# Optimization experiments

Hardware: AMD Instinct MI355X
Metric: run time of the kernel (lower is better)

## Reference

```python
import jax, jax.numpy as jnp
import numpy as np

NHEAD = 8  # matches init_kwargs

M_NODES = 20000
D_MODEL = 512
N_EDGES = 640000


def setup_inputs() -> dict:
    key = jax.random.key(0)
    ks = jax.random.split(key, 8)
    sc = 1.0 / np.sqrt(D_MODEL)
    return {
        "s": jax.random.normal(ks[0], (M_NODES, D_MODEL), dtype=jnp.float32),
        "edge_index": jax.random.randint(ks[1], (2, N_EDGES), 0, M_NODES, dtype=jnp.int64),
        "Wq": jax.random.normal(ks[2], (D_MODEL, D_MODEL), dtype=jnp.float32) * sc,
        "bq": jax.random.normal(ks[3], (D_MODEL,), dtype=jnp.float32) * sc,
        "Wkv": jax.random.normal(ks[4], (2 * D_MODEL, D_MODEL), dtype=jnp.float32) * sc,
        "bkv": jax.random.normal(ks[5], (2 * D_MODEL,), dtype=jnp.float32) * sc,
        "Wo": jax.random.normal(ks[6], (D_MODEL, D_MODEL), dtype=jnp.float32) * sc,
        "bo": jax.random.normal(ks[7], (D_MODEL,), dtype=jnp.float32) * sc,
    }


def reference(s, edge_index, Wq, bq, Wkv, bkv, Wo, bo):
    M, C = s.shape
    H = NHEAD
    Dh = C // H
    scale = 1.0 / np.sqrt(Dh).astype(np.float32)

    q = (s @ Wq.T + bq).reshape(M, H, Dh)            # [M,H,Dh]
    kv = (s @ Wkv.T + bkv).reshape(M, H, 2 * Dh)     # [M,H,2Dh]
    k, v = kv[..., :Dh], kv[..., Dh:]

    src, tgt = edge_index[0], edge_index[1]

    # per-edge attention logits [E,H]
    a = jnp.einsum('ehc,ehc->eh', q[tgt], k[src]) * scale

    # segment softmax over edges sharing the same target node
    a_max = jax.ops.segment_max(a, tgt, num_segments=M)        # [M,H]
    ex = jnp.exp(a - a_max[tgt])                               # [E,H]
    denom = jax.ops.segment_sum(ex, tgt, num_segments=M)      # [M,H]
    attn = ex / denom[tgt]                                     # [E,H]

    # weighted message aggregation: scatter-sum over target nodes
    o_msg = attn[..., None] * v[src]                           # [E,H,Dh]
    o = jax.ops.segment_sum(o_msg, tgt, num_segments=M)       # [M,H,Dh]
    o = o.reshape(M, C)
    return o @ Wo.T + bo
```

## Files before the change

### kernel.cpp

```cpp
#include <hip/hip_runtime.h>
#include <cmath>

#define MN 20000
#define DM 512
#define NE 640000
#define CAP 128

typedef short bf16x8 __attribute__((ext_vector_type(8)));
typedef float f32x4 __attribute__((ext_vector_type(4)));
typedef int   i32x4 __attribute__((ext_vector_type(4)));

__device__ __forceinline__ ushort f2b(float x) {
    unsigned u = __builtin_bit_cast(unsigned, x);
    u += 0x7FFF + ((u >> 16) & 1);
    return (ushort)(u >> 16);
}
__device__ __forceinline__ float b2f(ushort b) {
    return __builtin_bit_cast(float, (unsigned)b << 16);
}

#define NS4   (MN * DM / 4)
#define NWC4  (1536 * 512 / 4)
#define NWO4  (512 * 512 / 4)
#define NB4   (1536 / 4)

__device__ __forceinline__ const float* wc_src_row(int r, const float* Wq, const float* Wkv) {
    if (r < 512) return Wq + ((size_t)r << 9);
    if (r < 1024) { int h = (r - 512) >> 6, j = (r - 512) & 63;  return Wkv + ((size_t)(h * 128 + j) << 9); }
    { int h = (r - 1024) >> 6, j = (r - 1024) & 63; return Wkv + ((size_t)(h * 128 + 64 + j) << 9); }
}

__global__ void conv_all_k(const float* __restrict__ s, const float* __restrict__ Wq,
                           const float* __restrict__ Wkv, const float* __restrict__ Wo,
                           const float* __restrict__ bq, const float* __restrict__ bkv,
                           ushort* __restrict__ s_b, ushort* __restrict__ Wc_b,
                           ushort* __restrict__ Wo_b, float* __restrict__ bc)
{
    int i = blockIdx.x * blockDim.x + threadIdx.x;
    if (i < NS4) {
        float4 v = ((const float4*)s)[i];
        ushort4 o = { f2b(v.x), f2b(v.y), f2b(v.z), f2b(v.w) };
        ((ushort4*)s_b)[i] = o;
        return;
    }
    i -= NS4;
    if (i < NWC4) {
        int e = i * 4, row = e >> 9, col = e & 511;
        float4 v = *(const float4*)(wc_src_row(row, Wq, Wkv) + col);
        ushort4 o = { f2b(v.x), f2b(v.y), f2b(v.z), f2b(v.w) };
        ((ushort4*)Wc_b)[i] = o;
        return;
    }
    i -= NWC4;
    if (i < NWO4) {
        float4 v = ((const float4*)Wo)[i];
        ushort4 o = { f2b(v.x), f2b(v.y), f2b(v.z), f2b(v.w) };
        ((ushort4*)Wo_b)[i] = o;
        return;
    }
    i -= NWO4;
    if (i < NB4) {
#pragma unroll
        for (int u = 0; u < 4; ++u) {
            int r = i * 4 + u;
            float v;
            if (r < 512) v = bq[r];
            else if (r < 1024) { int h = (r - 512) >> 6, j = (r - 512) & 63;  v = bkv[h * 128 + j]; }
            else               { int h = (r - 1024) >> 6, j = (r - 1024) & 63; v = bkv[h * 128 + 64 + j]; }
            bc[r] = v;
        }
    }
}

template<int SPLIT, bool OUTBF>
__global__ __launch_bounds__(256) void gemm_mfma(
    const ushort* __restrict__ Ah, const ushort* __restrict__ Al,
    const ushort* __restrict__ Bh, const ushort* __restrict__ Bl,
    const float* __restrict__ bias, void* __restrict__ Cout, int M, int N, int K)
{
    __shared__ ushort lds[4 * 4096];
    const int tid = threadIdx.x;
    const int row0 = blockIdx.x * 128, col0 = blockIdx.y * 128;
    const int wid = tid >> 6, l = tid & 63;
    const int wm = (wid >> 1) * 64, wn = (wid & 1) * 64;
    const int fr = l & 15, g = l >> 4;
    const int fcb = g << 4;

    f32x4 acc[4][4] = {};

    for (int k0 = 0; k0 < K; k0 += 32) {
        __syncthreads();
#pragma unroll
        for (int c = 0; c < 2; ++c) {
            const int lb  = c * 4096 + tid * 16;
            const int r   = lb >> 6;
            const int cbs = (lb & 63) ^ ((r & 6) << 3);
            const int ar  = min(row0 + r, M - 1);
            const int br  = col0 + r;
            const size_t aoff = (size_t)ar * K + k0 + (cbs >> 1);
            const size_t boff = (size_t)br * K + k0 + (cbs >> 1);
            __builtin_amdgcn_global_load_lds(
                (const __attribute__((address_space(1))) void*)(Ah + aoff),
                (__attribute__((address_space(3))) void*)&lds[0 * 4096 + (lb >> 1)], 16, 0, 0);
            __builtin_amdgcn_global_load_lds(
                (const __attribute__((address_space(1))) void*)(Bh + boff),
                (__attribute__((address_space(3))) void*)&lds[1 * 4096 + (lb >> 1)], 16, 0, 0);
            if (SPLIT == 3) {
                __builtin_amdgcn_global_load_lds(
                    (const __attribute__((address_space(1))) void*)(Al + aoff),
                    (__attribute__((address_space(3))) void*)&lds[2 * 4096 + (lb >> 1)], 16, 0, 0);
                __builtin_amdgcn_global_load_lds(
                    (const __attribute__((address_space(1))) void*)(Bl + boff),
                    (__attribute__((address_space(3))) void*)&lds[3 * 4096 + (lb >> 1)], 16, 0, 0);
            }
        }
        __syncthreads();

        bf16x8 ah[4], bh[4], al[4], bl[4];
#pragma unroll
        for (int m = 0; m < 4; ++m) {
            const int r  = wm + m * 16 + fr;
            const int cb = fcb ^ ((r & 6) << 3);
            ah[m] = *(const bf16x8*)&lds[0 * 4096 + r * 32 + (cb >> 1)];
            if (SPLIT == 3) al[m] = *(const bf16x8*)&lds[2 * 4096 + r * 32 + (cb >> 1)];
        }
#pragma unroll
        for (int n = 0; n < 4; ++n) {
            const int r  = wn + n * 16 + fr;
            const int cb = fcb ^ ((r & 6) << 3);
            bh[n] = *(const bf16x8*)&lds[1 * 4096 + r * 32 + (cb >> 1)];
            if (SPLIT == 3) bl[n] = *(const bf16x8*)&lds[3 * 4096 + r * 32 + (cb >> 1)];
        }
#pragma unroll
        for (int m = 0; m < 4; ++m)
#pragma unroll
            for (int n = 0; n < 4; ++n) {
                acc[m][n] = __builtin_amdgcn_mfma_f32_16x16x32_bf16(ah[m], bh[n], acc[m][n], 0, 0, 0);
                if (SPLIT == 3) {
                    acc[m][n] = __builtin_amdgcn_mfma_f32_16x16x32_bf16(ah[m], bl[n], acc[m][n], 0, 0, 0);
                    acc[m][n] = __builtin_amdgcn_mfma_f32_16x16x32_bf16(al[m], bh[n], acc[m][n], 0, 0, 0);
                }
            }
    }

#pragma unroll
    for (int n = 0; n < 4; ++n) {
        const int cg = col0 + wn + n * 16 + fr;
        const float bv = bias[cg];
#pragma unroll
        for (int m = 0; m < 4; ++m) {
#pragma unroll
            for (int j = 0; j < 4; ++j) {
                const int rg = row0 + wm + m * 16 + g * 4 + j;
                if (rg < M) {
                    const float v = acc[m][n][j] + bv;
                    if (OUTBF) ((ushort*)Cout)[(size_t)rg * N + cg] = f2b(v);
                    else       ((float*)Cout)[(size_t)rg * N + cg] = v;
                }
            }
        }
    }
}

__global__ void count_edges_k(const int* __restrict__ tgt, int* __restrict__ counts, int E)
{
    int e = blockIdx.x * blockDim.x + threadIdx.x;
    if (e < E) atomicAdd(&counts[tgt[e]], 1);
}

__global__ __launch_bounds__(1024) void scan_counts_k(
    const int* __restrict__ counts, int* __restrict__ indptr,
    int* __restrict__ dbase, int M)
{
    __shared__ int part[1024];
    __shared__ int hist[128];
    const int t  = threadIdx.x;
    if (t < 128) hist[t] = 0;
    __syncthreads();
    const int CH = (M + 1023) / 1024;
    const int base = t * CH;
    int sum = 0;
    for (int i = 0; i < CH; ++i) {
        int idx = base + i;
        if (idx < M) {
            int c = counts[idx];
            sum += c;
            atomicAdd(&hist[127 - min(c, 127)], 1);
        }
    }
    part[t] = sum;
    __syncthreads();
    for (int off = 1; off < 1024; off <<= 1) {
        int v = (t >= off) ? part[t - off] : 0;
        __syncthreads();
        part[t] += v;
        __syncthreads();
    }
    int excl = part[t] - sum;
    for (int i = 0; i < CH; ++i) {
        int idx = base + i;
        if (idx < M) { indptr[idx] = excl; excl += counts[idx]; }
    }
    if (t == 1023) indptr[M] = part[1023];
    __syncthreads();
    if (t == 0) {
        int run = 0;
        for (int b = 0; b < 128; ++b) { int v = hist[b]; dbase[b] = run; run += v; }
    }
}

__global__ void scatter_fused_k(const int* __restrict__ src, const int* __restrict__ tgt,
                                const int* __restrict__ indptr, int* __restrict__ cursor,
                                int* __restrict__ slot_off, const int* __restrict__ counts,
                                const int* __restrict__ dbase, int* __restrict__ dcur,
                                int* __restrict__ perm, int E, int M)
{
    int e = blockIdx.x * blockDim.x + threadIdx.x;
    if (e < E) {
        int t   = tgt[e];
        int pos = atomicAdd(&cursor[t], 1);
        slot_off[indptr[t] + pos] = src[e] * 3072;
    }
    if (e < M) {
        int b = 127 - min(counts[e], 127);
        int pos = atomicAdd(&dcur[b], 1);
        perm[dbase[b] + pos] = e;
    }
}

__global__ __launch_bounds__(256, 3) void attn7_k(
    const ushort* __restrict__ qkv, const int* __restrict__ indptr,
    const int* __restrict__ slot_off, const int* __restrict__ perm,
    ushort* __restrict__ obh)
{
    __shared__ int slots[4][CAP];
    const int w = threadIdx.x >> 6;
    const int l = threadIdx.x & 63;
    const int node = perm[blockIdx.x * 4 + w];
    const int beg = indptr[node], end = indptr[node + 1];
    const int d = end - beg;
    const int dc = min(d, CAP);

    for (int i = l; i < dc; i += 64) slots[w][i] = slot_off[beg + i];
    __syncthreads();

    const char* base = (const char*)qkv + (l << 4);

    float qf[8];
    {
        bf16x8 qv = *(const bf16x8*)((const char*)qkv + (size_t)node * 3072 + (l << 4));
#pragma unroll
        for (int j = 0; j < 8; ++j) qf[j] = b2f((ushort)qv[j]);
    }

    float acc[8] = {};
    float ssum = 0.f;

    int i = 0;
    for (; i + 8 <= dc; i += 8) {
        const int4 sa = *(const int4*)&slots[w][i];
        const int4 sb = *(const int4*)&slots[w][i + 4];
        const char* bp[8] = { base + sa.x, base + sa.y, base + sa.z, base + sa.w,
                              base + sb.x, base + sb.y, base + sb.z, base + sb.w };
        i32x4 kr[8], vr[8];
#pragma unroll
        for (int u = 0; u < 8; ++u)
            asm volatile("global_load_dwordx4 %0, %1, off offset:1024"
                         : "=v"(kr[u]) : "v"(bp[u]));
#pragma unroll
        for (int u = 0; u < 8; ++u)
            asm volatile("global_load_dwordx4 %0, %1, off offset:2048"
                         : "=v"(vr[u]) : "v"(bp[u]));

        asm volatile("s_waitcnt vmcnt(8)" ::: "memory");
        __builtin_amdgcn_sched_barrier(0);

        float p[8];
#pragma unroll
        for (int u = 0; u < 8; ++u) {
            const bf16x8 kv = __builtin_bit_cast(bf16x8, kr[u]);
            float pu = 0.f;
#pragma unroll
            for (int j = 0; j < 8; ++j) pu = fmaf(qf[j], b2f((ushort)kv[j]), pu);
            p[u] = pu;
        }
#pragma unroll
        for (int u = 0; u < 8; ++u) p[u] += __shfl_xor(p[u], 1);
#pragma unroll
        for (int u = 0; u < 8; ++u) p[u] += __shfl_xor(p[u], 2);
#pragma unroll
        for (int u = 0; u < 8; ++u) p[u] += __shfl_xor(p[u], 4);
        float wt[8];
#pragma unroll
        for (int u = 0; u < 8; ++u) { wt[u] = __expf(p[u] * 0.125f); ssum += wt[u]; }

        asm volatile("s_waitcnt vmcnt(0)" ::: "memory");
        __builtin_amdgcn_sched_barrier(0);

#pragma unroll
        for (int u = 0; u < 8; ++u) {
            const bf16x8 vv = __builtin_bit_cast(bf16x8, vr[u]);
#pragma unroll
            for (int j = 0; j < 8; ++j) acc[j] = fmaf(wt[u], b2f((ushort)vv[j]), acc[j]);
        }
    }
    for (; i < d; ++i) {
        const int so = (i < CAP) ? slots[w][i] : slot_off[beg + i];
        const char* b0 = base + so;
        bf16x8 k0 = *(const bf16x8*)(b0 + 1024);
        bf16x8 v0 = *(const bf16x8*)(b0 + 2048);
        float p0 = 0.f;
#pragma unroll
        for (int j = 0; j < 8; ++j) p0 = fmaf(qf[j], b2f((ushort)k0[j]), p0);
        p0 += __shfl_xor(p0, 1); p0 += __shfl_xor(p0, 2); p0 += __shfl_xor(p0, 4);
        const float w0 = __expf(p0 * 0.125f);
        ssum += w0;
#pragma unroll
        for (int j = 0; j < 8; ++j) acc[j] = fmaf(w0, b2f((ushort)v0[j]), acc[j]);
    }

    const float inv = (d > 0) ? 1.f / ssum : 0.f;
    ushort4 ph0, ph1;
    ph0.x = f2b(acc[0] * inv); ph0.y = f2b(acc[1] * inv);
    ph0.z = f2b(acc[2] * inv); ph0.w = f2b(acc[3] * inv);
    ph1.x = f2b(acc[4] * inv); ph1.y = f2b(acc[5] * inv);
    ph1.z = f2b(acc[6] * inv); ph1.w = f2b(acc[7] * inv);
    const size_t ob_off = (size_t)node * 512 + (l << 3);
    *(ushort4*)(obh + ob_off)     = ph0;
    *(ushort4*)(obh + ob_off + 4) = ph1;
}

extern "C" void kernel_launch(void* const* d_in, const int* in_sizes, int n_in,
                              void* d_out, int out_size, void* d_ws, size_t ws_size,
                              hipStream_t stream)
{
    const float* s   = (const float*)d_in[0];
    const int*   eix = (const int*)d_in[1];
    const float* Wq  = (const float*)d_in[2];
    const float* bq  = (const float*)d_in[3];
    const float* Wkv = (const float*)d_in[4];
    const float* bkv = (const float*)d_in[5];
    const float* Wo  = (const float*)d_in[6];
    const float* bo  = (const float*)d_in[7];
    float* out = (float*)d_out;

    char* ws = (char*)d_ws;
    auto take = [&](size_t bytes) { char* p = ws; ws += (bytes + 255) & ~(size_t)255; return p; };
    ushort* qkv_b = (ushort*)take((size_t)MN * 1536 * 2);
    ushort* s_b   = (ushort*)take((size_t)MN * 512 * 2);
    ushort* obh   = (ushort*)take((size_t)MN * 512 * 2);
    ushort* Wc_b  = (ushort*)take((size_t)1536 * 512 * 2);
    ushort* Wo_b  = (ushort*)take((size_t)512 * 512 * 2);
    float*  bc    = (float*)take(1536 * 4);
    int* counts   = (int*)take(MN * 4);
    int* cursor   = (int*)take(MN * 4);
    int* slot_off = (int*)take((size_t)NE * 4);
    int* indptr   = (int*)take((MN + 4) * 4);
    int* dbase    = (int*)take(128 * 4);
    int* dcur     = (int*)take(128 * 4);
    int* perm     = (int*)take(MN * 4);

    hipMemsetAsync(counts, 0, MN * 4, stream);
    hipMemsetAsync(cursor, 0, MN * 4, stream);
    hipMemsetAsync(dcur, 0, 128 * 4, stream);

    const int convN = NS4 + NWC4 + NWO4 + NB4;
    conv_all_k<<<(convN + 255) / 256, 256, 0, stream>>>(s, Wq, Wkv, Wo, bq, bkv,
                                                        s_b, Wc_b, Wo_b, bc);

    count_edges_k<<<NE / 256, 256, 0, stream>>>(eix + NE, counts, NE);
    scan_counts_k<<<1, 1024, 0, stream>>>(counts, indptr, dbase, MN);
    scatter_fused_k<<<NE / 256, 256, 0, stream>>>(eix, eix + NE, indptr, cursor,
                                                  slot_off, counts, dbase, dcur, perm, NE, MN);

    dim3 g1((MN + 127) / 128, 1536 / 128);
    gemm_mfma<1, true><<<g1, 256, 0, stream>>>(s_b, s_b, Wc_b, Wc_b, bc, qkv_b, MN, 1536, DM);

    attn7_k<<<MN / 4, 256, 0, stream>>>(qkv_b, indptr, slot_off, perm, obh);

    dim3 g2((MN + 127) / 128, 512 / 128);
    gemm_mfma<1, false><<<g2, 256, 0, stream>>>(obh, obh, Wo_b, Wo_b, bo, out, MN, 512, DM);
}
```

Before: 428.9 us.

## Bucket edges by source tile and process five nodes per wave in tile order

Edges are now sub-sorted per target node into 20 buckets by source-node range (src>>10), using a second count array, a per-node tile offset kernel, and bucketed scatter. The attention kernel gives each wave five nodes and walks the source tiles in lockstep across them, so K/V rows gathered by concurrently running waves fall in the same source range and should get better L2/MALL reuse. In exchange it drops the 8-way batched asm loads and shared-memory slot staging for a simple one-edge-at-a-time loop with less memory-level parallelism, adds extra atomics and kernel launches, and makes the indptr2 sentinel depend on every edge target being valid.

```diff
diff --git a/kernel.cpp b/kernel.cpp
--- a/kernel.cpp
+++ b/kernel.cpp
@@ -4,11 +4,13 @@
 #define MN 20000
 #define DM 512
 #define NE 640000
-#define CAP 128
+#define NT 20
+#define TSHIFT 10
+#define NPW 5
+#define NWAVE 4000
 
 typedef short bf16x8 __attribute__((ext_vector_type(8)));
 typedef float f32x4 __attribute__((ext_vector_type(4)));
-typedef int   i32x4 __attribute__((ext_vector_type(4)));
 
 __device__ __forceinline__ ushort f2b(float x) {
     unsigned u = __builtin_bit_cast(unsigned, x);
@@ -162,10 +164,15 @@
     }
 }
 
-__global__ void count_edges_k(const int* __restrict__ tgt, int* __restrict__ counts, int E)
+__global__ void count_edges_k(const int* __restrict__ src, const int* __restrict__ tgt,
+                              int* __restrict__ counts, int* __restrict__ counts2, int E)
 {
     int e = blockIdx.x * blockDim.x + threadIdx.x;
-    if (e < E) atomicAdd(&counts[tgt[e]], 1);
+    if (e < E) {
+        int t = tgt[e];
+        atomicAdd(&counts[t], 1);
+        atomicAdd(&counts2[t * NT + (src[e] >> TSHIFT)], 1);
+    }
 }
 
 __global__ __launch_bounds__(1024) void scan_counts_k(
@@ -209,17 +216,31 @@
     }
 }
 
+__global__ void tileoff_k(const int* __restrict__ indptr, const int* __restrict__ counts2,
+                          int* __restrict__ indptr2, int* __restrict__ cursor2, int M)
+{
+    int n = blockIdx.x * blockDim.x + threadIdx.x;
+    if (n >= M) return;
+    int run = indptr[n];
+#pragma unroll
+    for (int j = 0; j < NT; ++j) {
+        indptr2[n * NT + j] = run;
+        cursor2[n * NT + j] = run;
+        run += counts2[n * NT + j];
+    }
+    if (n == 0) indptr2[M * NT] = NE;
+}
+
 __global__ void scatter_fused_k(const int* __restrict__ src, const int* __restrict__ tgt,
-                                const int* __restrict__ indptr, int* __restrict__ cursor,
-                                int* __restrict__ slot_off, const int* __restrict__ counts,
-                                const int* __restrict__ dbase, int* __restrict__ dcur,
-                                int* __restrict__ perm, int E, int M)
+                                int* __restrict__ cursor2, int* __restrict__ slot_off,
+                                const int* __restrict__ counts, const int* __restrict__ dbase,
+                                int* __restrict__ dcur, int* __restrict__ perm, int E, int M)
 {
     int e = blockIdx.x * blockDim.x + threadIdx.x;
     if (e < E) {
-        int t   = tgt[e];
-        int pos = atomicAdd(&cursor[t], 1);
-        slot_off[indptr[t] + pos] = src[e] * 3072;
+        int t = tgt[e], s = src[e];
+        int pos = atomicAdd(&cursor2[t * NT + (s >> TSHIFT)], 1);
+        slot_off[pos] = s * 3072;
     }
     if (e < M) {
         int b = 127 - min(counts[e], 127);
@@ -228,106 +249,64 @@
     }
 }
 
-__global__ __launch_bounds__(256, 3) void attn7_k(
-    const ushort* __restrict__ qkv, const int* __restrict__ indptr,
+__global__ __launch_bounds__(256, 4) void attn8_k(
+    const ushort* __restrict__ qkv, const int* __restrict__ indptr2,
     const int* __restrict__ slot_off, const int* __restrict__ perm,
     ushort* __restrict__ obh)
 {
-    __shared__ int slots[4][CAP];
-    const int w = threadIdx.x >> 6;
+    const int wave = (blockIdx.x * 256 + threadIdx.x) >> 6;
     const int l = threadIdx.x & 63;
-    const int node = perm[blockIdx.x * 4 + w];
-    const int beg = indptr[node], end = indptr[node + 1];
-    const int d = end - beg;
-    const int dc = min(d, CAP);
-
-    for (int i = l; i < dc; i += 64) slots[w][i] = slot_off[beg + i];
-    __syncthreads();
-
     const char* base = (const char*)qkv + (l << 4);
 
-    float qf[8];
-    {
-        bf16x8 qv = *(const bf16x8*)((const char*)qkv + (size_t)node * 3072 + (l << 4));
-#pragma unroll
-        for (int j = 0; j < 8; ++j) qf[j] = b2f((ushort)qv[j]);
-    }
-
-    float acc[8] = {};
-    float ssum = 0.f;
-
-    int i = 0;
-    for (; i + 8 <= dc; i += 8) {
-        const int4 sa = *(const int4*)&slots[w][i];
-        const int4 sb = *(const int4*)&slots[w][i + 4];
-        const char* bp[8] = { base + sa.x, base + sa.y, base + sa.z, base + sa.w,
-                              base + sb.x, base + sb.y, base + sb.z, base + sb.w };
-        i32x4 kr[8], vr[8];
-#pragma unroll
-        for (int u = 0; u < 8; ++u)
-            asm volatile("global_load_dwordx4 %0, %1, off offset:1024"
-                         : "=v"(kr[u]) : "v"(bp[u]));
-#pragma unroll
-        for (int u = 0; u < 8; ++u)
-            asm volatile("global_load_dwordx4 %0, %1, off offset:2048"
-                         : "=v"(vr[u]) : "v"(bp[u]));
-
-        asm volatile("s_waitcnt vmcnt(8)" ::: "memory");
-        __builtin_amdgcn_sched_barrier(0);
-
-        float p[8];
-#pragma unroll
-        for (int u = 0; u < 8; ++u) {
-            const bf16x8 kv = __builtin_bit_cast(bf16x8, kr[u]);
-            float pu = 0.f;
-#pragma unroll
-            for (int j = 0; j < 8; ++j) pu = fmaf(qf[j], b2f((ushort)kv[j]), pu);
-            p[u] = pu;
-        }
-#pragma unroll
-        for (int u = 0; u < 8; ++u) p[u] += __shfl_xor(p[u], 1);
-#pragma unroll
-        for (int u = 0; u < 8; ++u) p[u] += __shfl_xor(p[u], 2);
-#pragma unroll
-        for (int u = 0; u < 8; ++u) p[u] += __shfl_xor(p[u], 4);
-        float wt[8];
-#pragma unroll
-        for (int u = 0; u < 8; ++u) { wt[u] = __expf(p[u] * 0.125f); ssum += wt[u]; }
-
-        asm volatile("s_waitcnt vmcnt(0)" ::: "memory");
-        __builtin_amdgcn_sched_barrier(0);
-
-#pragma unroll
-        for (int u = 0; u < 8; ++u) {
-            const bf16x8 vv = __builtin_bit_cast(bf16x8, vr[u]);
-#pragma unroll
-            for (int j = 0; j < 8; ++j) acc[j] = fmaf(wt[u], b2f((ushort)vv[j]), acc[j]);
-        }
-    }
-    for (; i < d; ++i) {
-        const int so = (i < CAP) ? slots[w][i] : slot_off[beg + i];
-        const char* b0 = base + so;
-        bf16x8 k0 = *(const bf16x8*)(b0 + 1024);
-        bf16x8 v0 = *(const bf16x8*)(b0 + 2048);
-        float p0 = 0.f;
-#pragma unroll
-        for (int j = 0; j < 8; ++j) p0 = fmaf(qf[j], b2f((ushort)k0[j]), p0);
-        p0 += __shfl_xor(p0, 1); p0 += __shfl_xor(p0, 2); p0 += __shfl_xor(p0, 4);
-        const float w0 = __expf(p0 * 0.125f);
-        ssum += w0;
-#pragma unroll
-        for (int j = 0; j < 8; ++j) acc[j] = fmaf(w0, b2f((ushort)v0[j]), acc[j]);
-    }
-
-    const float inv = (d > 0) ? 1.f / ssum : 0.f;
-    ushort4 ph0, ph1;
-    ph0.x = f2b(acc[0] * inv); ph0.y = f2b(acc[1] * inv);
-    ph0.z = f2b(acc[2] * inv); ph0.w = f2b(acc[3] * inv);
-    ph1.x = f2b(acc[4] * inv); ph1.y = f2b(acc[5] * inv);
-    ph1.z = f2b(acc[6] * inv); ph1.w = f2b(acc[7] * inv);
-    const size_t ob_off = (size_t)node * 512 + (l << 3);
-    *(ushort4*)(obh + ob_off)     = ph0;
-    *(ushort4*)(obh + ob_off + 4) = ph1;
+    int node[NPW];
+#pragma unroll
+    for (int m = 0; m < NPW; ++m) node[m] = perm[m * NWAVE + wave];
+
+    float qf[NPW][8];
+#pragma unroll
+    for (int m = 0; m < NPW; ++m) {
+        bf16x8 qv = *(const bf16x8*)(base + (size_t)node[m] * 3072);
+#pragma unroll
+        for (int j = 0; j < 8; ++j) qf[m][j] = b2f((ushort)qv[j]);
+    }
+
+    float acc[NPW][8] = {};
+    float ssum[NPW] = {};
+
+    for (int j = 0; j < NT; ++j) {
+#pragma unroll
+        for (int m = 0; m < NPW; ++m) {
+            const int n20 = node[m] * NT + j;
+            const int b0 = indptr2[n20];
+            const int b1 = indptr2[n20 + 1];
+            for (int i = b0; i < b1; ++i) {
+                const char* bp = base + slot_off[i];
+                bf16x8 kv = *(const bf16x8*)(bp + 1024);
+                bf16x8 vv = *(const bf16x8*)(bp + 2048);
+                float p = 0.f;
+#pragma unroll
+                for (int t = 0; t < 8; ++t) p = fmaf(qf[m][t], b2f((ushort)kv[t]), p);
+                p += __shfl_xor(p, 1); p += __shfl_xor(p, 2); p += __shfl_xor(p, 4);
+                const float wgt = __expf(p * 0.125f);
+                ssum[m] += wgt;
+#pragma unroll
+                for (int t = 0; t < 8; ++t) acc[m][t] = fmaf(wgt, b2f((ushort)vv[t]), acc[m][t]);
+            }
+        }
+    }
+
+#pragma unroll
+    for (int m = 0; m < NPW; ++m) {
+        const float inv = (ssum[m] > 0.f) ? 1.f / ssum[m] : 0.f;
+        ushort4 ph0, ph1;
+        ph0.x = f2b(acc[m][0] * inv); ph0.y = f2b(acc[m][1] * inv);
+        ph0.z = f2b(acc[m][2] * inv); ph0.w = f2b(acc[m][3] * inv);
+        ph1.x = f2b(acc[m][4] * inv); ph1.y = f2b(acc[m][5] * inv);
+        ph1.z = f2b(acc[m][6] * inv); ph1.w = f2b(acc[m][7] * inv);
+        const size_t ob_off = (size_t)node[m] * 512 + (l << 3);
+        *(ushort4*)(obh + ob_off)     = ph0;
+        *(ushort4*)(obh + ob_off + 4) = ph1;
+    }
 }
 
 extern "C" void kernel_launch(void* const* d_in, const int* in_sizes, int n_in,
@@ -346,37 +325,40 @@
 
     char* ws = (char*)d_ws;
     auto take = [&](size_t bytes) { char* p = ws; ws += (bytes + 255) & ~(size_t)255; return p; };
-    ushort* qkv_b = (ushort*)take((size_t)MN * 1536 * 2);
-    ushort* s_b   = (ushort*)take((size_t)MN * 512 * 2);
-    ushort* obh   = (ushort*)take((size_t)MN * 512 * 2);
-    ushort* Wc_b  = (ushort*)take((size_t)1536 * 512 * 2);
-    ushort* Wo_b  = (ushort*)take((size_t)512 * 512 * 2);
-    float*  bc    = (float*)take(1536 * 4);
-    int* counts   = (int*)take(MN * 4);
-    int* cursor   = (int*)take(MN * 4);
-    int* slot_off = (int*)take((size_t)NE * 4);
-    int* indptr   = (int*)take((MN + 4) * 4);
-    int* dbase    = (int*)take(128 * 4);
-    int* dcur     = (int*)take(128 * 4);
-    int* perm     = (int*)take(MN * 4);
+    ushort* qkv_b  = (ushort*)take((size_t)MN * 1536 * 2);
+    ushort* s_b    = (ushort*)take((size_t)MN * 512 * 2);
+    ushort* obh    = (ushort*)take((size_t)MN * 512 * 2);
+    ushort* Wc_b   = (ushort*)take((size_t)1536 * 512 * 2);
+    ushort* Wo_b   = (ushort*)take((size_t)512 * 512 * 2);
+    float*  bc     = (float*)take(1536 * 4);
+    int* counts    = (int*)take(MN * 4);
+    int* counts2   = (int*)take((size_t)MN * NT * 4);
+    int* cursor2   = (int*)take((size_t)MN * NT * 4);
+    int* indptr2   = (int*)take(((size_t)MN * NT + 4) * 4);
+    int* slot_off  = (int*)take((size_t)NE * 4);
+    int* indptr    = (int*)take((MN + 4) * 4);
+    int* dbase     = (int*)take(128 * 4);
+    int* dcur      = (int*)take(128 * 4);
+    int* perm      = (int*)take(MN * 4);
 
     hipMemsetAsync(counts, 0, MN * 4, stream);
-    hipMemsetAsync(cursor, 0, MN * 4, stream);
+    hipMemsetAsync(counts2, 0, (size_t)MN * NT * 4, stream);
     hipMemsetAsync(dcur, 0, 128 * 4, stream);
 
     const int convN = NS4 + NWC4 + NWO4 + NB4;
     conv_all_k<<<(convN + 255) / 256, 256, 0, stream>>>(s, Wq, Wkv, Wo, bq, bkv,
                                                         s_b, Wc_b, Wo_b, bc);
 
-    count_edges_k<<<NE / 256, 256, 0, stream>>>(eix + NE, counts, NE);
+    count_edges_k<<<NE / 256, 256, 0, stream>>>(eix, eix + NE, counts, counts2, NE);
     scan_counts_k<<<1, 1024, 0, stream>>>(counts, indptr, dbase, MN);
-    scatter_fused_k<<<NE / 256, 256, 0, stream>>>(eix, eix + NE, indptr, cursor,
-                                                  slot_off, counts, dbase, dcur, perm, NE, MN);
+    tileoff_k<<<(MN + 255) / 256, 256, 0, stream>>>(indptr, counts2, indptr2, cursor2, MN);
+    scatter_fused_k<<<NE / 256, 256, 0, stream>>>(eix, eix + NE, cursor2, slot_off,
+                                                  counts, dbase, dcur, perm, NE, MN);
 
     dim3 g1((MN + 127) / 128, 1536 / 128);
     gemm_mfma<1, true><<<g1, 256, 0, stream>>>(s_b, s_b, Wc_b, Wc_b, bc, qkv_b, MN, 1536, DM);
 
-    attn7_k<<<MN / 4, 256, 0, stream>>>(qkv_b, indptr, slot_off, perm, obh);
+    attn8_k<<<NWAVE / 4, 256, 0, stream>>>(qkv_b, indptr2, slot_off, perm, obh);
 
     dim3 g2((MN + 127) / 128, 512 / 128);
     gemm_mfma<1, false><<<g2, 256, 0, stream>>>(obh, obh, Wo_b, Wo_b, bo, out, MN, 512, DM);
```

Measured after the change: 447.1 us. +4.2%, slower.
